# Optimization experiments

Hardware: AMD Instinct MI355X
Metric: run time of the kernel (lower is better)

Reference implementation:

```python
import jax, jax.numpy as jnp
import numpy as np

B, T, H, PRED = 16384, 8, 256, 12


def _cell(x, h, c, Wih, Whh, bih, bhh):
    # PyTorch LSTM gate order: i, f, g, o
    g = x @ Wih.T + h @ Whh.T + bih + bhh
    i, f, gg, o = jnp.split(g, 4, axis=-1)
    c = jax.nn.sigmoid(f) * c + jax.nn.sigmoid(i) * jnp.tanh(gg)
    h = jax.nn.sigmoid(o) * jnp.tanh(c)
    return h, c


def _run_seq(x, layers):
    # stacked LSTM over full sequence, zero initial state; x: [B, T, D]
    b = x.shape[0]
    inp = x
    hs, cs = [], []
    for (Wih, Whh, bih, bhh) in layers:
        h0 = jnp.zeros((b, Whh.shape[1]), x.dtype)

        def step(carry, xt, Wih=Wih, Whh=Whh, bih=bih, bhh=bhh):
            h, c = _cell(xt, carry[0], carry[1], Wih, Whh, bih, bhh)
            return (h, c), h

        (h, c), out = jax.lax.scan(step, (h0, h0), jnp.swapaxes(inp, 0, 1))
        inp = jnp.swapaxes(out, 0, 1)
        hs.append(h)
        cs.append(c)
    return inp, jnp.stack(hs), jnp.stack(cs)


def _step_stack(x, hs, cs, layers):
    # single-timestep pass through stacked LSTM; hs/cs: [L, B, H]
    inp = x
    nh, nc = [], []
    for l, (Wih, Whh, bih, bhh) in enumerate(layers):
        h, c = _cell(inp, hs[l], cs[l], Wih, Whh, bih, bhh)
        inp = h
        nh.append(h)
        nc.append(c)
    return inp, jnp.stack(nh), jnp.stack(nc)


def _forward(x, l1_Wih0, l1_Whh0, l1_bih0, l1_bhh0, l1_Wih1, l1_Whh1, l1_bih1, l1_bhh1,
             l2_Wih0, l2_Whh0, l2_bih0, l2_bhh0, l2_Wih1, l2_Whh1, l2_bih1, l2_bhh1,
             fc1_w, fc1_b, fc2_w, fc2_b):
    L1 = [(l1_Wih0, l1_Whh0, l1_bih0, l1_bhh0), (l1_Wih1, l1_Whh1, l1_bih1, l1_bhh1)]
    L2 = [(l2_Wih0, l2_Whh0, l2_bih0, l2_bhh0), (l2_Wih1, l2_Whh1, l2_bih1, l2_bhh1)]
    out1, h1, c1 = _run_seq(x, L1)           # encode observed track
    _, h2, c2 = _run_seq(out1, L2)
    pos = x[:, -1, :]

    def dec(carry, _):
        pos, h1, c1, h2, c2 = carry
        o1, h1, c1 = _step_stack(pos, h1, c1, L1)
        o2, h2, c2 = _step_stack(o1, h2, c2, L2)
        delta = jax.nn.relu(o2 @ fc1_w.T + fc1_b) @ fc2_w.T + fc2_b
        pos = pos + delta
        return (pos, h1, c1, h2, c2), pos

    _, preds = jax.lax.scan(dec, (pos, h1, c1, h2, c2), None, length=PRED)
    return jnp.swapaxes(preds, 0, 1)  # [B, PRED, 2]


def setup_inputs() -> dict:
    key = jax.random.key(0)
    ks = iter(jax.random.split(key, 32))
    s = 1.0 / np.sqrt(H)  # matches PyTorch LSTM/Linear init scale

    def mk(shape):
        return jax.random.uniform(next(ks), shape, jnp.float32, -s, s)

    d = {"x": jax.random.normal(next(ks), (B, T, 2), jnp.float32)}
    for name, in_dim in [("l1", 2), ("l2", H)]:
        for layer in range(2):
            di = in_dim if layer == 0 else H
            d[f"{name}_Wih{layer}"] = mk((4 * H, di))
            d[f"{name}_Whh{layer}"] = mk((4 * H, H))
            d[f"{name}_bih{layer}"] = mk((4 * H,))
            d[f"{name}_bhh{layer}"] = mk((4 * H,))
    d["fc1_w"] = mk((H, H))
    d["fc1_b"] = mk((H,))
    d["fc2_w"] = mk((2, H))
    d["fc2_b"] = mk((2,))
    return d


def reference(x, l1_Wih0, l1_Whh0, l1_bih0, l1_bhh0, l1_Wih1, l1_Whh1, l1_bih1, l1_bhh1,
              l2_Wih0, l2_Whh0, l2_bih0, l2_bhh0, l2_Wih1, l2_Whh1, l2_bih1, l2_bhh1,
              fc1_w, fc1_b, fc2_w, fc2_b):
    return _forward(x, l1_Wih0, l1_Whh0, l1_bih0, l1_bhh0, l1_Wih1, l1_Whh1, l1_bih1, l1_bhh1,
                    l2_Wih0, l2_Whh0, l2_bih0, l2_bhh0, l2_Wih1, l2_Whh1, l2_bih1, l2_bhh1,
                    fc1_w, fc1_b, fc2_w, fc2_b)
```

## Files before the change

kernel.cpp:

```cpp
#include <hip/hip_runtime.h>
#include <stdint.h>

#define Bsz   16384
#define Tseq  8
#define NPRED 12

typedef __attribute__((ext_vector_type(4))) float    f32x4;
typedef _Float16 h16;
typedef __attribute__((ext_vector_type(8))) _Float16 h16x8;

__device__ __forceinline__ float sigf(float x)   { return 1.f / (1.f + __expf(-x)); }
__device__ __forceinline__ float tanh_f(float x) { return 1.f - 2.f / (__expf(2.f * x) + 1.f); }

__device__ __forceinline__ void gload_lds16(const void* g, void* l) {
  __builtin_amdgcn_global_load_lds(
      (const __attribute__((address_space(1))) void*)g,
      (__attribute__((address_space(3))) void*)l, 16, 0, 0);
}

__global__ void zero_r7(f32x4* __restrict__ p, long n4) {
  long i = (long)blockIdx.x * 256 + threadIdx.x;
  f32x4 z; z[0] = 0.f; z[1] = 0.f; z[2] = 0.f; z[3] = 0.f;
  if (i < n4) p[i] = z;
}
__global__ void mark_r7(float* __restrict__ out) {
  if (blockIdx.x == 0 && threadIdx.x < 64) out[threadIdx.x] = 1000.0f;
}
__global__ void seed_r7(float* __restrict__ pos, const float* __restrict__ x) {
  int b = blockIdx.x * 256 + threadIdx.x;
  pos[2 * b]     = x[(size_t)b * 16 + 14];
  pos[2 * b + 1] = x[(size_t)b * 16 + 15];
}

__global__ void pack_w(h16* __restrict__ dst, const float* __restrict__ W0,
                       const float* __restrict__ W1, int ksplit, int Kw, int Np,
                       int gatePack) {
  int idx = blockIdx.x * 256 + threadIdx.x;
  if (idx >= Np * Kw) return;
  int np = idx / Kw, k = idx - np * Kw;
  int n = np;
  if (gatePack) { int jb = np >> 7, gi = (np >> 5) & 3, jr = np & 31; n = gi * 256 + jb * 32 + jr; }
  float w = (k < ksplit) ? W0[(size_t)n * ksplit + k]
                         : W1[(size_t)n * (Kw - ksplit) + (k - ksplit)];
  uint32_t byte = (uint32_t)np * (uint32_t)(Kw * 2) + (((uint32_t)k * 2) ^ (uint32_t)((np & 7) << 4));
  *(h16*)((char*)dst + byte) = (h16)w;
}

__global__ void add_bias(float* __restrict__ dst, const float* __restrict__ a,
                         const float* __restrict__ b) {
  int i = blockIdx.x * 256 + threadIdx.x;
  if (i < 1024) dst[i] = a[i] + b[i];
}

template <int NSEG, int HASX, int LSTM>
__global__ __launch_bounds__(256) void cell_gemm(
    const char* __restrict__ A0, const char* __restrict__ A1,
    const char* __restrict__ Wp, int Kw, int NY,
    const float* __restrict__ bias, const float* __restrict__ wih0,
    const float* __restrict__ xbase, int xstride,
    float* __restrict__ Cst, char* __restrict__ hout) {
  __shared__ __align__(16) char lds[32768];
  char* ldsA = lds;
  char* ldsB = lds + 16384;
  const int tid = threadIdx.x;
  const int wave = tid >> 6, lane = tid & 63;

  int lid = blockIdx.x;
  int chunkv = gridDim.x >> 3;
  int swz = (lid & 7) * chunkv + (lid >> 3);
  const int by = swz % NY, bx = swz / NY;
  const int m0 = bx * 128;
  const int n0 = by * 128;

  f32x4 acc[2][8];
#pragma unroll
  for (int m = 0; m < 2; m++)
#pragma unroll
    for (int n = 0; n < 8; n++)
#pragma unroll
      for (int e = 0; e < 4; e++) acc[m][n][e] = 0.f;

  const int rowa = tid >> 3;
  const int chb  = (tid & 7) * 16;
  const int KB   = Kw >> 6;

  for (int kb = 0; kb < KB; ++kb) {
    const char* Asrc; int k0;
    if (NSEG == 2 && kb >= 4) { Asrc = A1; k0 = (kb - 4) << 6; }
    else                      { Asrc = A0; k0 = kb << 6; }
#pragma unroll
    for (int it = 0; it < 4; ++it) {
      gload_lds16(Asrc + (size_t)(m0 + it * 32 + rowa) * 512 + k0 * 2 + chb,
                  ldsA + it * 4096 + wave * 1024);
      gload_lds16(Wp + (size_t)(n0 + it * 32 + rowa) * (Kw * 2) + kb * 128 + chb,
                  ldsB + it * 4096 + wave * 1024);
    }
    __syncthreads();
#pragma unroll
    for (int kk = 0; kk < 2; ++kk) {
      const int kbyte = kk * 64 + (lane >> 4) * 16;
      h16x8 af[2], bfr[8];
#pragma unroll
      for (int mt = 0; mt < 2; ++mt) {
        int r = wave * 32 + mt * 16 + (lane & 15);
        af[mt] = *(const h16x8*)(ldsA + r * 128 + (kbyte ^ ((r & 7) << 4)));
      }
#pragma unroll
      for (int nt = 0; nt < 8; ++nt) {
        int cc = nt * 16 + (lane & 15);
        bfr[nt] = *(const h16x8*)(ldsB + cc * 128 + (kbyte ^ ((cc & 7) << 4)));
      }
#pragma unroll
      for (int mt = 0; mt < 2; ++mt)
#pragma unroll
        for (int nt = 0; nt < 8; ++nt)
          acc[mt][nt] = __builtin_amdgcn_mfma_f32_16x16x32_f16(af[mt], bfr[nt], acc[mt][nt], 0, 0, 0);
    }
    __syncthreads();
  }

  if constexpr (LSTM) {
#pragma unroll
    for (int c = 0; c < 2; c++) {
      const int j = (n0 >> 2) + c * 16 + (lane & 15);
      const float bi = bias[j], bff = bias[256 + j], bg = bias[512 + j], bo = bias[768 + j];
      float wi0 = 0, wi1 = 0, wf0 = 0, wf1 = 0, wg0 = 0, wg1 = 0, wo0 = 0, wo1 = 0;
      if constexpr (HASX) {
        wi0 = wih0[2 * j];           wi1 = wih0[2 * j + 1];
        wf0 = wih0[2 * (256 + j)];   wf1 = wih0[2 * (256 + j) + 1];
        wg0 = wih0[2 * (512 + j)];   wg1 = wih0[2 * (512 + j) + 1];
        wo0 = wih0[2 * (768 + j)];   wo1 = wih0[2 * (768 + j) + 1];
      }
#pragma unroll
      for (int mt = 0; mt < 2; ++mt) {
#pragma unroll
        for (int e = 0; e < 4; e++) {
          const int b = m0 + wave * 32 + mt * 16 + (lane >> 4) * 4 + e;
          float vi = acc[mt][0 + c][e] + bi;
          float vf = acc[mt][2 + c][e] + bff;
          float vg = acc[mt][4 + c][e] + bg;
          float vo = acc[mt][6 + c][e] + bo;
          if constexpr (HASX) {
            const float x0 = xbase[(size_t)b * xstride];
            const float x1 = xbase[(size_t)b * xstride + 1];
            vi += x0 * wi0 + x1 * wi1;
            vf += x0 * wf0 + x1 * wf1;
            vg += x0 * wg0 + x1 * wg1;
            vo += x0 * wo0 + x1 * wo1;
          }
          const size_t ci = (size_t)b * 256 + j;
          float cn = sigf(vf) * Cst[ci] + sigf(vi) * tanh_f(vg);
          float h  = sigf(vo) * tanh_f(cn);
          Cst[ci] = cn;
          *(h16*)(hout + (size_t)b * 512 + (((unsigned)j * 2) ^ (unsigned)((b & 7) << 4))) = (h16)h;
        }
      }
    }
  } else {
#pragma unroll
    for (int nt = 0; nt < 8; ++nt) {
      const int n = n0 + nt * 16 + (lane & 15);
      const float bn = bias[n];
#pragma unroll
      for (int mt = 0; mt < 2; ++mt)
#pragma unroll
        for (int e = 0; e < 4; e++) {
          const int b = m0 + wave * 32 + mt * 16 + (lane >> 4) * 4 + e;
          float v = acc[mt][nt][e] + bn;
          v = v > 0.f ? v : 0.f;
          *(h16*)(hout + (size_t)b * 512 + (((unsigned)n * 2) ^ (unsigned)((b & 7) << 4))) = (h16)v;
        }
    }
  }
}

__global__ void fc2_pos(const char* __restrict__ r, const float* __restrict__ w,
                        const float* __restrict__ fb, float* __restrict__ pos,
                        float* __restrict__ out, int s) {
  int b = blockIdx.x * 256 + threadIdx.x;
  float a0 = fb[0], a1 = fb[1];
#pragma unroll
  for (int ch = 0; ch < 32; ch++) {
    h16x8 v = *(const h16x8*)(r + (size_t)b * 512 + (((unsigned)ch * 16) ^ (unsigned)((b & 7) << 4)));
#pragma unroll
    for (int e = 0; e < 8; e++) {
      float rv = (float)v[e];
      int k = ch * 8 + e;
      a0 += rv * w[k];
      a1 += rv * w[256 + k];
    }
  }
  float p0 = pos[2 * b] + a0;
  float p1 = pos[2 * b + 1] + a1;
  pos[2 * b] = p0;
  pos[2 * b + 1] = p1;
  out[(size_t)b * (NPRED * 2) + s * 2]     = p0;
  out[(size_t)b * (NPRED * 2) + s * 2 + 1] = p1;
}

extern "C" void kernel_launch(void* const* d_in, const int* in_sizes, int n_in,
                              void* d_out, int out_size, void* d_ws, size_t ws_size,
                              hipStream_t stream) {
  const float* x      = (const float*)d_in[0];
  const float* Wih[4] = {(const float*)d_in[1], (const float*)d_in[5],
                         (const float*)d_in[9], (const float*)d_in[13]};
  const float* Whh[4] = {(const float*)d_in[2], (const float*)d_in[6],
                         (const float*)d_in[10], (const float*)d_in[14]};
  const float* bih[4] = {(const float*)d_in[3], (const float*)d_in[7],
                         (const float*)d_in[11], (const float*)d_in[15]};
  const float* bhh[4] = {(const float*)d_in[4], (const float*)d_in[8],
                         (const float*)d_in[12], (const float*)d_in[16]};
  const float* fc1_w = (const float*)d_in[17];
  const float* fc1_b = (const float*)d_in[18];
  const float* fc2_w = (const float*)d_in[19];
  const float* fc2_b = (const float*)d_in[20];

  char* ws = (char*)d_ws;
  size_t off = 0;
  auto alloc = [&](size_t bytes) -> char* {
    char* p = ws + off;
    off += (bytes + 255) & ~(size_t)255;
    return p;
  };

  float* Cs[4];
  for (int l = 0; l < 4; l++) Cs[l] = (float*)alloc((size_t)Bsz * 256 * 4);
  char* zeroh = alloc((size_t)Bsz * 512);
  char* h10[2] = {alloc((size_t)Bsz * 512), alloc((size_t)Bsz * 512)};
  char* sl[2]  = {alloc((size_t)Bsz * 512), alloc((size_t)Bsz * 512)};
  char* h20[2] = {alloc((size_t)Bsz * 512), alloc((size_t)Bsz * 512)};
  char* h21[2] = {alloc((size_t)Bsz * 512), alloc((size_t)Bsz * 512)};
  char* rbuf = alloc((size_t)Bsz * 512);
  float* pos = (float*)alloc((size_t)Bsz * 2 * 4);
  float* biasc = (float*)alloc(4 * 1024 * 4);
  h16* wp10 = (h16*)alloc((size_t)1024 * 256 * 2);
  h16* wp[3];
  for (int i = 0; i < 3; i++) wp[i] = (h16*)alloc((size_t)1024 * 512 * 2);
  h16* wpf1 = (h16*)alloc((size_t)256 * 256 * 2);

  if (ws_size < off) {
    mark_r7<<<dim3(1), dim3(64), 0, stream>>>((float*)d_out);
    return;
  }

  {
    long n4 = ((size_t)Bsz * 256 * 4 * 4 + (size_t)Bsz * 512) / 16;
    zero_r7<<<dim3((unsigned)((n4 + 255) / 256)), dim3(256), 0, stream>>>((f32x4*)Cs[0], n4);
  }
  seed_r7<<<dim3(Bsz / 256), dim3(256), 0, stream>>>(pos, x);

  pack_w<<<dim3((1024 * 256 + 255) / 256), dim3(256), 0, stream>>>(wp10, Whh[0], Whh[0], 256, 256, 1024, 1);
  pack_w<<<dim3((1024 * 512 + 255) / 256), dim3(256), 0, stream>>>(wp[0], Wih[1], Whh[1], 256, 512, 1024, 1);
  pack_w<<<dim3((1024 * 512 + 255) / 256), dim3(256), 0, stream>>>(wp[1], Wih[2], Whh[2], 256, 512, 1024, 1);
  pack_w<<<dim3((1024 * 512 + 255) / 256), dim3(256), 0, stream>>>(wp[2], Wih[3], Whh[3], 256, 512, 1024, 1);
  pack_w<<<dim3((256 * 256 + 255) / 256), dim3(256), 0, stream>>>(wpf1, fc1_w, fc1_w, 256, 256, 256, 0);
  for (int l = 0; l < 4; l++)
    add_bias<<<dim3(4), dim3(256), 0, stream>>>(biasc + l * 1024, bih[l], bhh[l]);

  for (int t = 0; t < Tseq; t++) {
    int cur = t & 1, prev = cur ^ 1;
    const char* h10r = (t == 0) ? zeroh : h10[prev];
    const char* slr  = (t == 0) ? zeroh : sl[prev];
    const char* h20r = (t == 0) ? zeroh : h20[prev];
    const char* h21r = (t == 0) ? zeroh : h21[prev];
    cell_gemm<1, 1, 1><<<dim3(1024), dim3(256), 0, stream>>>(
        h10r, zeroh, (const char*)wp10, 256, 8, biasc, Wih[0], x + t * 2, 16, Cs[0], h10[cur]);
    cell_gemm<2, 0, 1><<<dim3(1024), dim3(256), 0, stream>>>(
        h10[cur], slr, (const char*)wp[0], 512, 8, biasc + 1024, nullptr, nullptr, 0, Cs[1], sl[cur]);
    cell_gemm<2, 0, 1><<<dim3(1024), dim3(256), 0, stream>>>(
        sl[cur], h20r, (const char*)wp[1], 512, 8, biasc + 2048, nullptr, nullptr, 0, Cs[2], h20[cur]);
    cell_gemm<2, 0, 1><<<dim3(1024), dim3(256), 0, stream>>>(
        h20[cur], h21r, (const char*)wp[2], 512, 8, biasc + 3072, nullptr, nullptr, 0, Cs[3], h21[cur]);
  }

  for (int s = 0; s < NPRED; s++) {
    int u = Tseq + s, cur = u & 1, prev = cur ^ 1;
    cell_gemm<1, 1, 1><<<dim3(1024), dim3(256), 0, stream>>>(
        h10[prev], zeroh, (const char*)wp10, 256, 8, biasc, Wih[0], pos, 2, Cs[0], h10[cur]);
    cell_gemm<2, 0, 1><<<dim3(1024), dim3(256), 0, stream>>>(
        h10[cur], sl[prev], (const char*)wp[0], 512, 8, biasc + 1024, nullptr, nullptr, 0, Cs[1], sl[cur]);
    cell_gemm<2, 0, 1><<<dim3(1024), dim3(256), 0, stream>>>(
        sl[cur], h20[prev], (const char*)wp[1], 512, 8, biasc + 2048, nullptr, nullptr, 0, Cs[2], h20[cur]);
    cell_gemm<2, 0, 1><<<dim3(1024), dim3(256), 0, stream>>>(
        h20[cur], h21[prev], (const char*)wp[2], 512, 8, biasc + 3072, nullptr, nullptr, 0, Cs[3], h21[cur]);
    cell_gemm<1, 0, 0><<<dim3(256), dim3(256), 0, stream>>>(
        h21[cur], zeroh, (const char*)wpf1, 256, 2, fc1_b, nullptr, nullptr, 0, nullptr, rbuf);
    fc2_pos<<<dim3(Bsz / 256), dim3(256), 0, stream>>>(rbuf, fc2_w, fc2_b, pos, (float*)d_out, s);
  }
}
```

Before: 2.788 ms.

## Fuse whole LSTM encoder/decoder into one persistent batch-row kernel

Replaces the ~100 per-step GEMM kernel launches with a single kernel. Each 512-thread block owns 64 batch rows and walks every timestep, layer and the FC head for them, so no grid-wide sync is needed. Weights are repacked into tile-contiguous blocks and streamed through double-buffered LDS. Other changes: cell state is stored in fp16, the t=0 layer-0 step is computed analytically without a GEMM, the zero-state matmuls at t=0 are skipped, and fc2 is fused into the head. The trade-offs are lower fp16 precision for the cell state and re-reading all weights from L2 for every 64-row block, with only 256 blocks available as parallelism.

```diff
diff --git a/kernel.cpp b/kernel.cpp
--- a/kernel.cpp
+++ b/kernel.cpp
@@ -4,6 +4,7 @@
 #define Bsz   16384
 #define Tseq  8
 #define NPRED 12
+#define RPB   64
 
 typedef __attribute__((ext_vector_type(4))) float    f32x4;
 typedef _Float16 h16;
@@ -18,18 +19,8 @@
       (__attribute__((address_space(3))) void*)l, 16, 0, 0);
 }
 
-__global__ void zero_r7(f32x4* __restrict__ p, long n4) {
-  long i = (long)blockIdx.x * 256 + threadIdx.x;
-  f32x4 z; z[0] = 0.f; z[1] = 0.f; z[2] = 0.f; z[3] = 0.f;
-  if (i < n4) p[i] = z;
-}
-__global__ void mark_r7(float* __restrict__ out) {
+__global__ void mark_r14(float* __restrict__ out) {
   if (blockIdx.x == 0 && threadIdx.x < 64) out[threadIdx.x] = 1000.0f;
-}
-__global__ void seed_r7(float* __restrict__ pos, const float* __restrict__ x) {
-  int b = blockIdx.x * 256 + threadIdx.x;
-  pos[2 * b]     = x[(size_t)b * 16 + 14];
-  pos[2 * b + 1] = x[(size_t)b * 16 + 15];
 }
 
 __global__ void pack_w(h16* __restrict__ dst, const float* __restrict__ W0,
@@ -38,11 +29,17 @@
   int idx = blockIdx.x * 256 + threadIdx.x;
   if (idx >= Np * Kw) return;
   int np = idx / Kw, k = idx - np * Kw;
+  int nb = np >> 8, r = np & 255;
   int n = np;
-  if (gatePack) { int jb = np >> 7, gi = (np >> 5) & 3, jr = np & 31; n = gi * 256 + jb * 32 + jr; }
+  if (gatePack) {
+    int wcq = r >> 6, gi = (r >> 4) & 3, jr = r & 15;
+    n = gi * 256 + nb * 64 + wcq * 16 + jr;
+  }
   float w = (k < ksplit) ? W0[(size_t)n * ksplit + k]
                          : W1[(size_t)n * (Kw - ksplit) + (k - ksplit)];
-  uint32_t byte = (uint32_t)np * (uint32_t)(Kw * 2) + (((uint32_t)k * 2) ^ (uint32_t)((np & 7) << 4));
+  int KB = Kw >> 6, kb = k >> 6;
+  uint32_t byte = (uint32_t)(nb * KB + kb) * 32768u + (uint32_t)r * 128u
+                + ((2u * (uint32_t)(k & 63)) ^ (uint32_t)((r & 7) << 4));
   *(h16*)((char*)dst + byte) = (h16)w;
 }
 
@@ -52,150 +49,223 @@
   if (i < 1024) dst[i] = a[i] + b[i];
 }
 
-template <int NSEG, int HASX, int LSTM>
-__global__ __launch_bounds__(256) void cell_gemm(
-    const char* __restrict__ A0, const char* __restrict__ A1,
-    const char* __restrict__ Wp, int Kw, int NY,
-    const float* __restrict__ bias, const float* __restrict__ wih0,
-    const float* __restrict__ xbase, int xstride,
-    float* __restrict__ Cst, char* __restrict__ hout) {
-  __shared__ __align__(16) char lds[32768];
-  char* ldsA = lds;
-  char* ldsB = lds + 16384;
-  const int tid = threadIdx.x;
+__device__ __forceinline__ void gemm_tile(
+    const char* A0, const char* A1, const char* wTile, int KBiter,
+    int m0, char* lds, int tid, f32x4 acc[2][4]) {
   const int wave = tid >> 6, lane = tid & 63;
-
-  int lid = blockIdx.x;
-  int chunkv = gridDim.x >> 3;
-  int swz = (lid & 7) * chunkv + (lid >> 3);
-  const int by = swz % NY, bx = swz / NY;
-  const int m0 = bx * 128;
-  const int n0 = by * 128;
-
-  f32x4 acc[2][8];
+  const int wr = wave >> 2, wc = wave & 3;
+
 #pragma unroll
   for (int m = 0; m < 2; m++)
 #pragma unroll
-    for (int n = 0; n < 8; n++)
+    for (int n = 0; n < 4; n++)
 #pragma unroll
       for (int e = 0; e < 4; e++) acc[m][n][e] = 0.f;
 
-  const int rowa = tid >> 3;
-  const int chb  = (tid & 7) * 16;
-  const int KB   = Kw >> 6;
-
-  for (int kb = 0; kb < KB; ++kb) {
-    const char* Asrc; int k0;
-    if (NSEG == 2 && kb >= 4) { Asrc = A1; k0 = (kb - 4) << 6; }
-    else                      { Asrc = A0; k0 = kb << 6; }
-#pragma unroll
-    for (int it = 0; it < 4; ++it) {
-      gload_lds16(Asrc + (size_t)(m0 + it * 32 + rowa) * 512 + k0 * 2 + chb,
-                  ldsA + it * 4096 + wave * 1024);
-      gload_lds16(Wp + (size_t)(n0 + it * 32 + rowa) * (Kw * 2) + kb * 128 + chb,
-                  ldsB + it * 4096 + wave * 1024);
-    }
+  const char* aP0 = A0 + (size_t)(m0 + (tid >> 3)) * 512 + (tid & 7) * 16;
+  const char* aP1 = A1 + (size_t)(m0 + (tid >> 3)) * 512 + (tid & 7) * 16;
+
+  auto STAGE = [&](int bsel, int kb) {
+    char* bufA = lds + bsel * 41216;
+    char* bufW = bufA + 8192;
+    const char* asrc = (KBiter == 8)
+        ? (kb < 4 ? aP0 + kb * 128 : aP1 + (kb - 4) * 128)
+        : aP0 + kb * 128;
+    gload_lds16(asrc, bufA + wave * 1024);
+    const char* wsrc = wTile + (size_t)kb * 32768 + wave * 1024 + lane * 16;
+#pragma unroll
+    for (int it = 0; it < 4; ++it)
+      gload_lds16(wsrc + it * 8192, bufW + it * 8192 + wave * 1024);
+  };
+
+  __syncthreads();
+  STAGE(0, 0);
+  for (int kb = 0; kb < KBiter; ++kb) {
     __syncthreads();
+    if (kb + 1 < KBiter) STAGE((kb + 1) & 1, kb + 1);
+    char* bufA = lds + (kb & 1) * 41216;
+    char* bufW = bufA + 8192;
 #pragma unroll
     for (int kk = 0; kk < 2; ++kk) {
       const int kbyte = kk * 64 + (lane >> 4) * 16;
-      h16x8 af[2], bfr[8];
+      h16x8 af[2], bfr[4];
 #pragma unroll
       for (int mt = 0; mt < 2; ++mt) {
-        int r = wave * 32 + mt * 16 + (lane & 15);
-        af[mt] = *(const h16x8*)(ldsA + r * 128 + (kbyte ^ ((r & 7) << 4)));
+        int r = wr * 32 + mt * 16 + (lane & 15);
+        af[mt] = *(const h16x8*)(bufA + r * 128 + (kbyte ^ ((r & 7) << 4)));
       }
 #pragma unroll
-      for (int nt = 0; nt < 8; ++nt) {
-        int cc = nt * 16 + (lane & 15);
-        bfr[nt] = *(const h16x8*)(ldsB + cc * 128 + (kbyte ^ ((cc & 7) << 4)));
+      for (int nt = 0; nt < 4; ++nt) {
+        int c = wc * 64 + nt * 16 + (lane & 15);
+        bfr[nt] = *(const h16x8*)(bufW + c * 128 + (kbyte ^ ((c & 7) << 4)));
       }
 #pragma unroll
       for (int mt = 0; mt < 2; ++mt)
 #pragma unroll
-        for (int nt = 0; nt < 8; ++nt)
+        for (int nt = 0; nt < 4; ++nt)
           acc[mt][nt] = __builtin_amdgcn_mfma_f32_16x16x32_f16(af[mt], bfr[nt], acc[mt][nt], 0, 0, 0);
     }
-    __syncthreads();
-  }
-
-  if constexpr (LSTM) {
-#pragma unroll
-    for (int c = 0; c < 2; c++) {
-      const int j = (n0 >> 2) + c * 16 + (lane & 15);
-      const float bi = bias[j], bff = bias[256 + j], bg = bias[512 + j], bo = bias[768 + j];
-      float wi0 = 0, wi1 = 0, wf0 = 0, wf1 = 0, wg0 = 0, wg1 = 0, wo0 = 0, wo1 = 0;
-      if constexpr (HASX) {
-        wi0 = wih0[2 * j];           wi1 = wih0[2 * j + 1];
-        wf0 = wih0[2 * (256 + j)];   wf1 = wih0[2 * (256 + j) + 1];
-        wg0 = wih0[2 * (512 + j)];   wg1 = wih0[2 * (512 + j) + 1];
-        wo0 = wih0[2 * (768 + j)];   wo1 = wih0[2 * (768 + j) + 1];
+  }
+}
+
+__device__ __forceinline__ void lstm_ep(
+    f32x4 acc[2][4], int m0, int nb, int tid, const float* bias,
+    const float* wih0x, const float* xbase, int xstride, int hasx, int skipc,
+    h16* Cst, char* hout) {
+  const int wave = tid >> 6, lane = tid & 63;
+  const int wr = wave >> 2, wc = wave & 3;
+  const int j = nb * 64 + wc * 16 + (lane & 15);
+  const float bi = bias[j], bff = bias[256 + j], bg = bias[512 + j], bo = bias[768 + j];
+  float wi0 = 0, wi1 = 0, wf0 = 0, wf1 = 0, wg0 = 0, wg1 = 0, wo0 = 0, wo1 = 0;
+  if (hasx) {
+    wi0 = wih0x[2 * j];           wi1 = wih0x[2 * j + 1];
+    wf0 = wih0x[2 * (256 + j)];   wf1 = wih0x[2 * (256 + j) + 1];
+    wg0 = wih0x[2 * (512 + j)];   wg1 = wih0x[2 * (512 + j) + 1];
+    wo0 = wih0x[2 * (768 + j)];   wo1 = wih0x[2 * (768 + j) + 1];
+  }
+#pragma unroll
+  for (int mt = 0; mt < 2; ++mt) {
+#pragma unroll
+    for (int e = 0; e < 4; e++) {
+      const int b = m0 + wr * 32 + mt * 16 + (lane >> 4) * 4 + e;
+      float vi = acc[mt][0][e] + bi;
+      float vf = acc[mt][1][e] + bff;
+      float vg = acc[mt][2][e] + bg;
+      float vo = acc[mt][3][e] + bo;
+      if (hasx) {
+        const float x0 = xbase[(size_t)b * xstride];
+        const float x1 = xbase[(size_t)b * xstride + 1];
+        vi += x0 * wi0 + x1 * wi1;
+        vf += x0 * wf0 + x1 * wf1;
+        vg += x0 * wg0 + x1 * wg1;
+        vo += x0 * wo0 + x1 * wo1;
       }
-#pragma unroll
-      for (int mt = 0; mt < 2; ++mt) {
-#pragma unroll
-        for (int e = 0; e < 4; e++) {
-          const int b = m0 + wave * 32 + mt * 16 + (lane >> 4) * 4 + e;
-          float vi = acc[mt][0 + c][e] + bi;
-          float vf = acc[mt][2 + c][e] + bff;
-          float vg = acc[mt][4 + c][e] + bg;
-          float vo = acc[mt][6 + c][e] + bo;
-          if constexpr (HASX) {
-            const float x0 = xbase[(size_t)b * xstride];
-            const float x1 = xbase[(size_t)b * xstride + 1];
-            vi += x0 * wi0 + x1 * wi1;
-            vf += x0 * wf0 + x1 * wf1;
-            vg += x0 * wg0 + x1 * wg1;
-            vo += x0 * wo0 + x1 * wo1;
-          }
-          const size_t ci = (size_t)b * 256 + j;
-          float cn = sigf(vf) * Cst[ci] + sigf(vi) * tanh_f(vg);
-          float h  = sigf(vo) * tanh_f(cn);
-          Cst[ci] = cn;
-          *(h16*)(hout + (size_t)b * 512 + (((unsigned)j * 2) ^ (unsigned)((b & 7) << 4))) = (h16)h;
-        }
+      const size_t ci = (size_t)b * 256 + j;
+      float cn = sigf(vi) * tanh_f(vg);
+      if (!skipc) cn += sigf(vf) * (float)Cst[ci];
+      float h = sigf(vo) * tanh_f(cn);
+      Cst[ci] = (h16)cn;
+      *(h16*)(hout + (size_t)b * 512 + (((unsigned)j * 2) ^ (unsigned)((b & 7) << 4))) = (h16)h;
+    }
+  }
+}
+
+__device__ void cell_block(const char* A0, const char* A1, const char* Wp,
+                           int KBiter, int KBpack,
+                           const float* bias, const float* wih0x, const float* xbase,
+                           int xstride, int hasx, int skipc,
+                           h16* Cst, char* hout, int m0, char* lds, int tid) {
+  for (int nb = 0; nb < 4; ++nb) {
+    f32x4 acc[2][4];
+    gemm_tile(A0, A1, Wp + (size_t)nb * KBpack * 32768, KBiter, m0, lds, tid, acc);
+    lstm_ep(acc, m0, nb, tid, bias, wih0x, xbase, xstride, hasx, skipc, Cst, hout);
+  }
+}
+
+__device__ void l0t0_block(const float* x, const float* wih0, const float* bias,
+                           h16* C, char* hout, int m0, int tid) {
+  const int r = tid & 63, jg = tid >> 6;
+  const size_t b = (size_t)(m0 + r);
+  const float x0 = x[b * 16], x1 = x[b * 16 + 1];
+#pragma unroll
+  for (int q = 0; q < 4; ++q) {
+    const int j0 = jg * 32 + q * 8;
+    h16 cc[8], hh[8];
+#pragma unroll
+    for (int u = 0; u < 8; ++u) {
+      int j = j0 + u;
+      float vi = bias[j]       + x0 * wih0[2 * j]         + x1 * wih0[2 * j + 1];
+      float vg = bias[512 + j] + x0 * wih0[2 * (512 + j)] + x1 * wih0[2 * (512 + j) + 1];
+      float vo = bias[768 + j] + x0 * wih0[2 * (768 + j)] + x1 * wih0[2 * (768 + j) + 1];
+      float cn = sigf(vi) * tanh_f(vg);
+      hh[u] = (h16)(sigf(vo) * tanh_f(cn));
+      cc[u] = (h16)cn;
+    }
+    *(h16x8*)(C + b * 256 + j0) = *(h16x8*)cc;
+    *(h16x8*)(hout + b * 512 + (((unsigned)j0 * 2) ^ (unsigned)((b & 7) << 4))) = *(h16x8*)hh;
+  }
+}
+
+__device__ void head_block(const char* A, const char* wpf1, const float* b1,
+                           const float* w2, const float* b2, float* pos, float* out,
+                           int s, int m0, char* lds, int tid) {
+  f32x4 acc[2][4];
+  gemm_tile(A, A, wpf1, 4, m0, lds, tid, acc);
+  __syncthreads();
+  h16* strip = (h16*)lds;
+  const int wave = tid >> 6, lane = tid & 63;
+  const int wr = wave >> 2, wc = wave & 3;
+#pragma unroll
+  for (int nt = 0; nt < 4; ++nt) {
+    const int n = wc * 64 + nt * 16 + (lane & 15);
+    const float bn = b1[n];
+#pragma unroll
+    for (int mt = 0; mt < 2; ++mt)
+#pragma unroll
+      for (int e = 0; e < 4; ++e) {
+        const int bl = wr * 32 + mt * 16 + (lane >> 4) * 4 + e;
+        float v = acc[mt][nt][e] + bn;
+        strip[bl * 262 + n] = (h16)(v > 0.f ? v : 0.f);
       }
-    }
-  } else {
-#pragma unroll
-    for (int nt = 0; nt < 8; ++nt) {
-      const int n = n0 + nt * 16 + (lane & 15);
-      const float bn = bias[n];
-#pragma unroll
-      for (int mt = 0; mt < 2; ++mt)
-#pragma unroll
-        for (int e = 0; e < 4; e++) {
-          const int b = m0 + wave * 32 + mt * 16 + (lane >> 4) * 4 + e;
-          float v = acc[mt][nt][e] + bn;
-          v = v > 0.f ? v : 0.f;
-          *(h16*)(hout + (size_t)b * 512 + (((unsigned)n * 2) ^ (unsigned)((b & 7) << 4))) = (h16)v;
-        }
-    }
-  }
-}
-
-__global__ void fc2_pos(const char* __restrict__ r, const float* __restrict__ w,
-                        const float* __restrict__ fb, float* __restrict__ pos,
-                        float* __restrict__ out, int s) {
-  int b = blockIdx.x * 256 + threadIdx.x;
-  float a0 = fb[0], a1 = fb[1];
-#pragma unroll
-  for (int ch = 0; ch < 32; ch++) {
-    h16x8 v = *(const h16x8*)(r + (size_t)b * 512 + (((unsigned)ch * 16) ^ (unsigned)((b & 7) << 4)));
-#pragma unroll
-    for (int e = 0; e < 8; e++) {
-      float rv = (float)v[e];
-      int k = ch * 8 + e;
-      a0 += rv * w[k];
-      a1 += rv * w[256 + k];
-    }
-  }
-  float p0 = pos[2 * b] + a0;
-  float p1 = pos[2 * b + 1] + a1;
-  pos[2 * b] = p0;
-  pos[2 * b + 1] = p1;
-  out[(size_t)b * (NPRED * 2) + s * 2]     = p0;
-  out[(size_t)b * (NPRED * 2) + s * 2 + 1] = p1;
+  }
+  __syncthreads();
+  if (tid < 128) {
+    const int bl2 = tid >> 1, comp = tid & 1;
+    const float* wrow = w2 + comp * 256;
+    float a = 0.f;
+#pragma unroll 8
+    for (int n = 0; n < 256; ++n) a += (float)strip[bl2 * 262 + n] * wrow[n];
+    const size_t b = (size_t)(m0 + bl2);
+    float p = pos[2 * b + comp] + a + b2[comp];
+    pos[2 * b + comp] = p;
+    out[b * (NPRED * 2) + s * 2 + comp] = p;
+  }
+  __syncthreads();
+}
+
+struct AllArgs {
+  const float* x;
+  const float* wih0;
+  const char* wp10; const char* wp0; const char* wp1; const char* wp2; const char* wpf1;
+  const float* biasc;
+  const float* fc1_b; const float* fc2_w; const float* fc2_b;
+  char* h0[2]; char* h1[2]; char* h2[2]; char* h3[2];
+  h16* C0; h16* C1; h16* C2; h16* C3;
+  float* pos;
+  float* out;
+};
+
+__global__ __launch_bounds__(512, 2) void lstm_all(AllArgs a) {
+  __shared__ __align__(16) char lds[84992];
+  const int tid = threadIdx.x;
+  const int m0 = blockIdx.x * RPB;
+
+  if (tid < 128) {
+    const size_t b = (size_t)(m0 + (tid >> 1));
+    a.pos[2 * b + (tid & 1)] = a.x[b * 16 + 14 + (tid & 1)];
+  }
+
+  l0t0_block(a.x, a.wih0, a.biasc, a.C0, a.h0[0], m0, tid);
+  cell_block(a.h0[0], a.h0[0], a.wp0, 4, 8, a.biasc + 1024, nullptr, nullptr, 0, 0, 1, a.C1, a.h1[0], m0, lds, tid);
+  cell_block(a.h1[0], a.h1[0], a.wp1, 4, 8, a.biasc + 2048, nullptr, nullptr, 0, 0, 1, a.C2, a.h2[0], m0, lds, tid);
+  cell_block(a.h2[0], a.h2[0], a.wp2, 4, 8, a.biasc + 3072, nullptr, nullptr, 0, 0, 1, a.C3, a.h3[0], m0, lds, tid);
+
+  for (int t = 1; t < Tseq; ++t) {
+    const int cur = t & 1, prev = cur ^ 1;
+    cell_block(a.h0[prev], a.h0[prev], a.wp10, 4, 4, a.biasc, a.wih0, a.x + t * 2, 16, 1, 0, a.C0, a.h0[cur], m0, lds, tid);
+    cell_block(a.h0[cur], a.h1[prev], a.wp0, 8, 8, a.biasc + 1024, nullptr, nullptr, 0, 0, 0, a.C1, a.h1[cur], m0, lds, tid);
+    cell_block(a.h1[cur], a.h2[prev], a.wp1, 8, 8, a.biasc + 2048, nullptr, nullptr, 0, 0, 0, a.C2, a.h2[cur], m0, lds, tid);
+    cell_block(a.h2[cur], a.h3[prev], a.wp2, 8, 8, a.biasc + 3072, nullptr, nullptr, 0, 0, 0, a.C3, a.h3[cur], m0, lds, tid);
+  }
+
+  for (int s = 0; s < NPRED; ++s) {
+    const int u = Tseq + s, cur = u & 1, prev = cur ^ 1;
+    cell_block(a.h0[prev], a.h0[prev], a.wp10, 4, 4, a.biasc, a.wih0, a.pos, 2, 1, 0, a.C0, a.h0[cur], m0, lds, tid);
+    cell_block(a.h0[cur], a.h1[prev], a.wp0, 8, 8, a.biasc + 1024, nullptr, nullptr, 0, 0, 0, a.C1, a.h1[cur], m0, lds, tid);
+    cell_block(a.h1[cur], a.h2[prev], a.wp1, 8, 8, a.biasc + 2048, nullptr, nullptr, 0, 0, 0, a.C2, a.h2[cur], m0, lds, tid);
+    cell_block(a.h2[cur], a.h3[prev], a.wp2, 8, 8, a.biasc + 3072, nullptr, nullptr, 0, 0, 0, a.C3, a.h3[cur], m0, lds, tid);
+    head_block(a.h3[cur], a.wpf1, a.fc1_b, a.fc2_w, a.fc2_b, a.pos, a.out, s, m0, lds, tid);
+  }
 }
 
 extern "C" void kernel_launch(void* const* d_in, const int* in_sizes, int n_in,
@@ -223,14 +293,13 @@
     return p;
   };
 
-  float* Cs[4];
-  for (int l = 0; l < 4; l++) Cs[l] = (float*)alloc((size_t)Bsz * 256 * 4);
-  char* zeroh = alloc((size_t)Bsz * 512);
-  char* h10[2] = {alloc((size_t)Bsz * 512), alloc((size_t)Bsz * 512)};
-  char* sl[2]  = {alloc((size_t)Bsz * 512), alloc((size_t)Bsz * 512)};
-  char* h20[2] = {alloc((size_t)Bsz * 512), alloc((size_t)Bsz * 512)};
-  char* h21[2] = {alloc((size_t)Bsz * 512), alloc((size_t)Bsz * 512)};
-  char* rbuf = alloc((size_t)Bsz * 512);
+  h16* Cs[4];
+  for (int l = 0; l < 4; l++) Cs[l] = (h16*)alloc((size_t)Bsz * 256 * 2);
+  char* hb[4][2];
+  for (int l = 0; l < 4; l++) {
+    hb[l][0] = alloc((size_t)Bsz * 512);
+    hb[l][1] = alloc((size_t)Bsz * 512);
+  }
   float* pos = (float*)alloc((size_t)Bsz * 2 * 4);
   float* biasc = (float*)alloc(4 * 1024 * 4);
   h16* wp10 = (h16*)alloc((size_t)1024 * 256 * 2);
@@ -239,15 +308,9 @@
   h16* wpf1 = (h16*)alloc((size_t)256 * 256 * 2);
 
   if (ws_size < off) {
-    mark_r7<<<dim3(1), dim3(64), 0, stream>>>((float*)d_out);
+    mark_r14<<<dim3(1), dim3(64), 0, stream>>>((float*)d_out);
     return;
   }
-
-  {
-    long n4 = ((size_t)Bsz * 256 * 4 * 4 + (size_t)Bsz * 512) / 16;
-    zero_r7<<<dim3((unsigned)((n4 + 255) / 256)), dim3(256), 0, stream>>>((f32x4*)Cs[0], n4);
-  }
-  seed_r7<<<dim3(Bsz / 256), dim3(256), 0, stream>>>(pos, x);
 
   pack_w<<<dim3((1024 * 256 + 255) / 256), dim3(256), 0, stream>>>(wp10, Whh[0], Whh[0], 256, 256, 1024, 1);
   pack_w<<<dim3((1024 * 512 + 255) / 256), dim3(256), 0, stream>>>(wp[0], Wih[1], Whh[1], 256, 512, 1024, 1);
@@ -257,34 +320,18 @@
   for (int l = 0; l < 4; l++)
     add_bias<<<dim3(4), dim3(256), 0, stream>>>(biasc + l * 1024, bih[l], bhh[l]);
 
-  for (int t = 0; t < Tseq; t++) {
-    int cur = t & 1, prev = cur ^ 1;
-    const char* h10r = (t == 0) ? zeroh : h10[prev];
-    const char* slr  = (t == 0) ? zeroh : sl[prev];
-    const char* h20r = (t == 0) ? zeroh : h20[prev];
-    const char* h21r = (t == 0) ? zeroh : h21[prev];
-    cell_gemm<1, 1, 1><<<dim3(1024), dim3(256), 0, stream>>>(
-        h10r, zeroh, (const char*)wp10, 256, 8, biasc, Wih[0], x + t * 2, 16, Cs[0], h10[cur]);
-    cell_gemm<2, 0, 1><<<dim3(1024), dim3(256), 0, stream>>>(
-        h10[cur], slr, (const char*)wp[0], 512, 8, biasc + 1024, nullptr, nullptr, 0, Cs[1], sl[cur]);
-    cell_gemm<2, 0, 1><<<dim3(1024), dim3(256), 0, stream>>>(
-        sl[cur], h20r, (const char*)wp[1], 512, 8, biasc + 2048, nullptr, nullptr, 0, Cs[2], h20[cur]);
-    cell_gemm<2, 0, 1><<<dim3(1024), dim3(256), 0, stream>>>(
-        h20[cur], h21r, (const char*)wp[2], 512, 8, biasc + 3072, nullptr, nullptr, 0, Cs[3], h21[cur]);
-  }
-
-  for (int s = 0; s < NPRED; s++) {
-    int u = Tseq + s, cur = u & 1, prev = cur ^ 1;
-    cell_gemm<1, 1, 1><<<dim3(1024), dim3(256), 0, stream>>>(
-        h10[prev], zeroh, (const char*)wp10, 256, 8, biasc, Wih[0], pos, 2, Cs[0], h10[cur]);
-    cell_gemm<2, 0, 1><<<dim3(1024), dim3(256), 0, stream>>>(
-        h10[cur], sl[prev], (const char*)wp[0], 512, 8, biasc + 1024, nullptr, nullptr, 0, Cs[1], sl[cur]);
-    cell_gemm<2, 0, 1><<<dim3(1024), dim3(256), 0, stream>>>(
-        sl[cur], h20[prev], (const char*)wp[1], 512, 8, biasc + 2048, nullptr, nullptr, 0, Cs[2], h20[cur]);
-    cell_gemm<2, 0, 1><<<dim3(1024), dim3(256), 0, stream>>>(
-        h20[cur], h21[prev], (const char*)wp[2], 512, 8, biasc + 3072, nullptr, nullptr, 0, Cs[3], h21[cur]);
-    cell_gemm<1, 0, 0><<<dim3(256), dim3(256), 0, stream>>>(
-        h21[cur], zeroh, (const char*)wpf1, 256, 2, fc1_b, nullptr, nullptr, 0, nullptr, rbuf);
-    fc2_pos<<<dim3(Bsz / 256), dim3(256), 0, stream>>>(rbuf, fc2_w, fc2_b, pos, (float*)d_out, s);
-  }
-}
+  AllArgs a;
+  a.x = x; a.wih0 = Wih[0];
+  a.wp10 = (const char*)wp10; a.wp0 = (const char*)wp[0];
+  a.wp1 = (const char*)wp[1]; a.wp2 = (const char*)wp[2];
+  a.wpf1 = (const char*)wpf1;
+  a.biasc = biasc;
+  a.fc1_b = fc1_b; a.fc2_w = fc2_w; a.fc2_b = fc2_b;
+  for (int l = 0; l < 2; l++) {
+    a.h0[l] = hb[0][l]; a.h1[l] = hb[1][l]; a.h2[l] = hb[2][l]; a.h3[l] = hb[3][l];
+  }
+  a.C0 = Cs[0]; a.C1 = Cs[1]; a.C2 = Cs[2]; a.C3 = Cs[3];
+  a.pos = pos; a.out = (float*)d_out;
+
+  lstm_all<<<dim3(Bsz / RPB), dim3(512), 0, stream>>>(a);
+}
```

New measurement: 3.053 ms. 1.09x slower.
